# Performance work log

Measured on AMD Instinct MI355X. Metric: run time of the kernel, lower is better.

Reference implementation:

```python
import jax, jax.numpy as jnp
import numpy as np

B, LQ, LK, C = 16, 1024, 1024, 512
WH = int(LQ ** 0.5)  # 32


def setup_inputs() -> dict:
    key = jax.random.key(0)
    ks = jax.random.split(key, 6)
    s1 = 1.0 / np.sqrt(LK)
    return {
        "query": jax.random.normal(ks[0], (B, LQ, C), jnp.float32),
        "key": jax.random.normal(ks[1], (B, LK, C), jnp.float32),
        "value": jax.random.normal(ks[2], (B, LK, C), jnp.float32),
        # nn.Linear weights, stored [out_features, in_features] like torch
        "w1": jax.random.normal(ks[3], (LK, LK), jnp.float32) * s1,
        "w2": jax.random.normal(ks[4], (LK, LK), jnp.float32) * s1,
        "w3": jax.random.normal(ks[5], (1, LK), jnp.float32) * s1,
    }


def reference(query, key, value, w1, w2, w3):
    # cosine-similarity matrix (computed under no_grad in the original)
    q = query / 100.0
    k = key / 100.0
    qn = jnp.sqrt(jnp.sum(q * q, axis=-1))[:, :, None]   # [B, LQ, 1]
    kn = jnp.sqrt(jnp.sum(k * k, axis=-1))[:, None, :]   # [B, 1, LK]
    outer = qn * kn                                       # rank-1 outer product [B, LQ, LK]
    upper = jnp.einsum('bqc,bkc->bqk', q, k)              # [B, LQ, LK]
    similar_rev = jax.lax.stop_gradient(upper / (outer + 1e-6))

    # 3-layer MLP gating over the LK axis -> scalar weight per query row
    h = jax.nn.gelu(jnp.einsum('bqk,ok->bqo', similar_rev, w1), approximate=False)
    h = jax.nn.gelu(jnp.einsum('bqk,ok->bqo', h, w2), approximate=False)
    w = jnp.einsum('bqk,ok->bqo', h, w3)[..., 0]          # [B, LQ]

    # weight^T @ similar_rev / wh, then tanh -> per-key scalar gate [B, LK, 1]
    weight = jnp.einsum('bq,bqk->bk', w, similar_rev) / WH
    weight = jnp.tanh(weight)[:, :, None]

    # value modulation + residual
    return value * weight + value
```

## Files before the change

### kernel.cpp

```cpp
#include <hip/hip_runtime.h>
#include <hip/hip_bf16.h>

#define B_  16
#define LQ_ 1024
#define LK_ 1024
#define C_  512

typedef __attribute__((ext_vector_type(4))) float f32x4;
typedef __attribute__((ext_vector_type(8))) short bf16x8;

__device__ __forceinline__ float bf2f(ushort u) {
  union { unsigned int i; float f; } v; v.i = ((unsigned int)u) << 16; return v.f;
}
__device__ __forceinline__ ushort f2bf(float f) {
  union { float f; unsigned int i; } v; v.f = f;
  unsigned int r = v.i + 0x7fffu + ((v.i >> 16) & 1u);
  return (ushort)(r >> 16);
}
__device__ __forceinline__ float gelu_exact(float x) {
  return 0.5f * x * (1.0f + erff(x * 0.70710678118654752f));
}

__device__ __forceinline__ void gload_lds16(const ushort* g, ushort* l) {
  __builtin_amdgcn_global_load_lds(
      (const __attribute__((address_space(1))) void*)g,
      (__attribute__((address_space(3))) void*)l, 16, 0, 0);
}

__global__ __launch_bounds__(256) void prep_qk(const float* __restrict__ x,
                                               ushort* __restrict__ xb,
                                               float* __restrict__ norms) {
  int wid = blockIdx.x * 4 + (threadIdx.x >> 6);
  int lane = threadIdx.x & 63;
  const float* xr = x + (long)wid * C_;
  ushort* xo = xb + (long)wid * C_;
  float ss = 0.f;
#pragma unroll
  for (int i0 = 0; i0 < 2; ++i0) {
    int i = lane * 4 + i0 * 256;
    float4 v = *(const float4*)(xr + i);
    ss += v.x * v.x + v.y * v.y + v.z * v.z + v.w * v.w;
    ushort4 o;
    o.x = f2bf(v.x); o.y = f2bf(v.y); o.z = f2bf(v.z); o.w = f2bf(v.w);
    *(ushort4*)(xo + i) = o;
  }
#pragma unroll
  for (int off = 32; off > 0; off >>= 1) ss += __shfl_xor(ss, off);
  if (lane == 0) norms[wid] = sqrtf(ss);
}

__global__ __launch_bounds__(256) void conv_bf16(const float* __restrict__ x,
                                                 ushort* __restrict__ o, int n4) {
  int i = blockIdx.x * 256 + threadIdx.x;
  if (i < n4) {
    float4 v = *(const float4*)(x + (long)i * 4);
    ushort4 u;
    u.x = f2bf(v.x); u.y = f2bf(v.y); u.z = f2bf(v.z); u.w = f2bf(v.w);
    *(ushort4*)(o + (long)i * 4) = u;
  }
}

template <int EPI>
__global__ __launch_bounds__(512, 2) void gemm256(
    const ushort* __restrict__ A, const ushort* __restrict__ Bm,
    ushort* __restrict__ Cc, int K, long sA, long sB, long sC,
    const float* __restrict__ qn, const float* __restrict__ kn,
    const float* __restrict__ w3v, float* __restrict__ wv) {
  int per = (int)(gridDim.x >> 3);
  int orig = blockIdx.x;
  int id = (orig & 7) * per + (orig >> 3);
  int b = id >> 4;
  int rt = id & 15;
  const int bm = (rt >> 2) * 256, bn = (rt & 3) * 256;

  A += (long)b * sA;
  Bm += (long)b * sB;

  __shared__ ushort At[2][256][64];
  __shared__ ushort Bt[2][256][64];
  const int bufStride = 256 * 64;

  const int tid = threadIdx.x;
  const int lane = tid & 63, w = tid >> 6;
  const int wr = w >> 2, wc = w & 3;
  const int l16 = lane & 15, lhi = lane >> 4;

  f32x4 acc[8][4] = {};

  const ushort* gA[4];
  const ushort* gB[4];
  ushort* lA[4];
  ushort* lB[4];
#pragma unroll
  for (int i = 0; i < 4; ++i) {
    int c = i * 512 + tid;
    int row = c >> 3;
    int cb = (c & 7) ^ (row & 7);
    gA[i] = A + (long)(bm + row) * K + cb * 8;
    gB[i] = Bm + (long)(bn + row) * K + cb * 8;
    int wch = i * 512 + (tid & ~63);
    lA[i] = &At[0][0][0] + (size_t)wch * 8;
    lB[i] = &Bt[0][0][0] + (size_t)wch * 8;
  }

#pragma unroll
  for (int i = 0; i < 4; ++i) {
    gload_lds16(gA[i], lA[i]);
    gload_lds16(gB[i], lB[i]);
  }
  asm volatile("s_waitcnt vmcnt(0)" ::: "memory");
  __builtin_amdgcn_s_barrier();

  const int nt = K / 64;
  int cur = 0;
  for (int t = 0; t < nt; ++t) {
    const int koff = (t + 1) * 64;
    const bool pf = (t + 1 < nt);
    const ushort* Acur = &At[cur][0][0];
    const ushort* Bcur = &Bt[cur][0][0];
    const size_t nxo = (size_t)(cur ^ 1) * bufStride;

    bf16x8 bfr[4][2];

#pragma unroll
    for (int p = 0; p < 4; ++p) {
      bf16x8 af[2][2];
#pragma unroll
      for (int e = 0; e < 2; ++e)
#pragma unroll
        for (int kk = 0; kk < 2; ++kk) {
          int r = wr * 128 + (p * 2 + e) * 16 + l16;
          af[e][kk] = *(const bf16x8*)(Acur + r * 64 +
                                       (((kk * 4 + lhi) ^ (r & 7)) * 8));
        }
      if (p == 0) {
#pragma unroll
        for (int n = 0; n < 4; ++n)
#pragma unroll
          for (int kk = 0; kk < 2; ++kk) {
            int r = wc * 64 + n * 16 + l16;
            bfr[n][kk] = *(const bf16x8*)(Bcur + r * 64 +
                                          (((kk * 4 + lhi) ^ (r & 7)) * 8));
          }
      }
      if (pf) {
        if (p == 0) {
          gload_lds16(gA[0] + koff, lA[0] + nxo);
          gload_lds16(gA[1] + koff, lA[1] + nxo);
          gload_lds16(gB[0] + koff, lB[0] + nxo);
        } else if (p == 1) {
          gload_lds16(gA[2] + koff, lA[2] + nxo);
          gload_lds16(gA[3] + koff, lA[3] + nxo);
          gload_lds16(gB[1] + koff, lB[1] + nxo);
        } else if (p == 2) {
          gload_lds16(gB[2] + koff, lB[2] + nxo);
          gload_lds16(gB[3] + koff, lB[3] + nxo);
        }
      }
      __builtin_amdgcn_s_barrier();
      __builtin_amdgcn_s_setprio(1);
#pragma unroll
      for (int e = 0; e < 2; ++e)
#pragma unroll
        for (int n = 0; n < 4; ++n)
#pragma unroll
          for (int kk = 0; kk < 2; ++kk)
            acc[p * 2 + e][n] = __builtin_amdgcn_mfma_f32_16x16x32_bf16(
                af[e][kk], bfr[n][kk], acc[p * 2 + e][n], 0, 0, 0);
      __builtin_amdgcn_s_setprio(0);
      if (p == 3) asm volatile("s_waitcnt vmcnt(0)" ::: "memory");
      __builtin_amdgcn_s_barrier();
    }
    cur ^= 1;
  }

  if constexpr (EPI == 2) {
    float* wvb = wv + (long)b * LQ_;
    float w3c[4];
#pragma unroll
    for (int n = 0; n < 4; ++n) w3c[n] = w3v[bn + wc * 64 + n * 16 + l16];
#pragma unroll
    for (int m = 0; m < 8; ++m)
#pragma unroll
      for (int rr = 0; rr < 4; ++rr) {
        float s = 0.f;
#pragma unroll
        for (int n = 0; n < 4; ++n)
          s += gelu_exact(acc[m][n][rr]) * w3c[n];
        s += __shfl_xor(s, 1);
        s += __shfl_xor(s, 2);
        s += __shfl_xor(s, 4);
        s += __shfl_xor(s, 8);
        if (l16 == 0)
          atomicAdd(&wvb[bm + wr * 128 + m * 16 + lhi * 4 + rr], s);
      }
  } else {
    Cc += (long)b * sC;
    const float* qnb = qn + (long)b * LQ_;
    const float* knb = kn + (long)b * LK_;
#pragma unroll
    for (int m = 0; m < 8; ++m) {
      int row0 = bm + wr * 128 + m * 16 + lhi * 4;
#pragma unroll
      for (int n = 0; n < 4; ++n) {
        int col = bn + wc * 64 + n * 16 + l16;
#pragma unroll
        for (int rr = 0; rr < 4; ++rr) {
          float v = acc[m][n][rr];
          int grow = row0 + rr;
          if (EPI == 0) {
            v = v / (qnb[grow] * knb[col] + 1e-2f);
          } else {
            v = gelu_exact(v);
          }
          Cc[(long)grow * 1024 + col] = f2bf(v);
        }
      }
    }
  }
}

__global__ __launch_bounds__(256) void gate_partial(const ushort* __restrict__ S,
                                                    const float* __restrict__ wv,
                                                    float* __restrict__ wraw) {
  int b = blockIdx.z;
  int k = blockIdx.x * 256 + threadIdx.x;
  int q0 = blockIdx.y * 128;
  const ushort* Sb = S + (long)b * LQ_ * LK_;
  const float* wb = wv + b * LQ_;
  float acc = 0.f;
#pragma unroll 4
  for (int q = q0; q < q0 + 128; ++q) acc += wb[q] * bf2f(Sb[(long)q * LK_ + k]);
  atomicAdd(&wraw[b * LK_ + k], acc);
}

__global__ __launch_bounds__(256) void finalize(const float* __restrict__ value,
                                                const float* __restrict__ wraw,
                                                float* __restrict__ out) {
  long i = (long)blockIdx.x * 256 + threadIdx.x;
  long e = i * 4;
  int row = (int)(e >> 9);
  float g = 1.f + tanhf(wraw[row] * (1.f / 32.f));
  float4 v = ((const float4*)value)[i];
  v.x *= g; v.y *= g; v.z *= g; v.w *= g;
  ((float4*)out)[i] = v;
}

extern "C" void kernel_launch(void* const* d_in, const int* in_sizes, int n_in,
                              void* d_out, int out_size, void* d_ws,
                              size_t ws_size, hipStream_t stream) {
  const float* query = (const float*)d_in[0];
  const float* key   = (const float*)d_in[1];
  const float* value = (const float*)d_in[2];
  const float* w1    = (const float*)d_in[3];
  const float* w2    = (const float*)d_in[4];
  const float* w3    = (const float*)d_in[5];
  float* out = (float*)d_out;

  const size_t QB_BYTES = (size_t)B_ * LQ_ * C_ * 2;
  const size_t S_BYTES  = (size_t)B_ * LQ_ * LK_ * 2;
  const size_t W_BYTES  = (size_t)LK_ * LK_ * 2;
  const size_t OFF_QB = 0;
  const size_t OFF_KB = OFF_QB + QB_BYTES;
  const size_t OFF_S  = OFF_KB + QB_BYTES;
  const size_t OFF_H1 = OFF_S + S_BYTES;
  const size_t OFF_W1 = OFF_H1 + S_BYTES;
  const size_t OFF_W2 = OFF_W1 + W_BYTES;
  const size_t OFF_QN = OFF_W2 + W_BYTES;
  const size_t OFF_KN = OFF_QN + (size_t)B_ * LQ_ * 4;
  const size_t OFF_WV = OFF_KN + (size_t)B_ * LK_ * 4;
  const size_t OFF_WR = OFF_WV + (size_t)B_ * LQ_ * 4;
  const size_t TOTAL  = OFF_WR + (size_t)B_ * LK_ * 4;
  if (ws_size < TOTAL) return;

  char* ws = (char*)d_ws;
  ushort* Qb  = (ushort*)(ws + OFF_QB);
  ushort* Kb  = (ushort*)(ws + OFF_KB);
  ushort* S   = (ushort*)(ws + OFF_S);
  ushort* h1  = (ushort*)(ws + OFF_H1);
  ushort* W1b = (ushort*)(ws + OFF_W1);
  ushort* W2b = (ushort*)(ws + OFF_W2);
  float* qn   = (float*)(ws + OFF_QN);
  float* kn   = (float*)(ws + OFF_KN);
  float* wv   = (float*)(ws + OFF_WV);
  float* wraw = (float*)(ws + OFF_WR);

  prep_qk<<<dim3(B_ * LQ_ / 4), 256, 0, stream>>>(query, Qb, qn);
  prep_qk<<<dim3(B_ * LK_ / 4), 256, 0, stream>>>(key, Kb, kn);
  conv_bf16<<<dim3(LK_ * LK_ / 4 / 256), 256, 0, stream>>>(w1, W1b, LK_ * LK_ / 4);
  conv_bf16<<<dim3(LK_ * LK_ / 4 / 256), 256, 0, stream>>>(w2, W2b, LK_ * LK_ / 4);
  hipMemsetAsync(wraw, 0, (size_t)B_ * LK_ * 4, stream);
  hipMemsetAsync(wv, 0, (size_t)B_ * LQ_ * 4, stream);

  gemm256<0><<<dim3(256), 512, 0, stream>>>(
      Qb, Kb, S, C_, (long)LQ_ * C_, (long)LK_ * C_, (long)LQ_ * LK_,
      qn, kn, nullptr, nullptr);

  gemm256<1><<<dim3(256), 512, 0, stream>>>(
      S, W1b, h1, LK_, (long)LQ_ * LK_, 0L, (long)LQ_ * LK_,
      nullptr, nullptr, nullptr, nullptr);

  gemm256<2><<<dim3(256), 512, 0, stream>>>(
      h1, W2b, nullptr, LK_, (long)LQ_ * LK_, 0L, 0L,
      nullptr, nullptr, w3, wv);

  gate_partial<<<dim3(LK_ / 256, LQ_ / 128, B_), 256, 0, stream>>>(S, wv, wraw);

  finalize<<<dim3((size_t)B_ * LK_ * C_ / 4 / 256), 256, 0, stream>>>(value, wraw, out);
}
```

Before: 170.2 us.

## Restructure GEMM main loop into four quadrant phases with finer-grained prefetch waits

Rewrites the 256x256 bf16 GEMM inner loop into four MFMA quadrants per k-tile. Each quadrant issues a pair of global-to-LDS prefetches, and the vmcnt waits are staggered so later loads stay in flight across phases instead of draining fully each tile. B rows are remapped so each wave's two n-halves sit in separate 128-row LDS regions, allowing B fragments to be loaded in halves. The aim is to overlap global loads, LDS reads and MFMA work more tightly. In exchange it depends on subtle vmcnt accounting and barrier placement to stay correct, and the epilogue's acc-to-column mapping must match the new B row permutation.

Measured after the change: 166.2 us. -2.3%, faster.

```diff
diff --git a/kernel.cpp b/kernel.cpp
--- a/kernel.cpp
+++ b/kernel.cpp
@@ -73,12 +73,11 @@
   int rt = id & 15;
   const int bm = (rt >> 2) * 256, bn = (rt & 3) * 256;
 
-  A += (long)b * sA;
+  A += (long)b * sA + (long)bm * K;
   Bm += (long)b * sB;
 
-  __shared__ ushort At[2][256][64];
-  __shared__ ushort Bt[2][256][64];
-  const int bufStride = 256 * 64;
+  __shared__ ushort At[2][256 * 64];
+  __shared__ ushort Bt[2][256 * 64];
 
   const int tid = threadIdx.x;
   const int lane = tid & 63, w = tid >> 6;
@@ -87,92 +86,130 @@
 
   f32x4 acc[8][4] = {};
 
-  const ushort* gA[4];
-  const ushort* gB[4];
-  ushort* lA[4];
-  ushort* lB[4];
-#pragma unroll
-  for (int i = 0; i < 4; ++i) {
-    int c = i * 512 + tid;
-    int row = c >> 3;
-    int cb = (c & 7) ^ (row & 7);
-    gA[i] = A + (long)(bm + row) * K + cb * 8;
-    gB[i] = Bm + (long)(bn + row) * K + cb * 8;
-    int wch = i * 512 + (tid & ~63);
-    lA[i] = &At[0][0][0] + (size_t)wch * 8;
-    lB[i] = &Bt[0][0][0] + (size_t)wch * 8;
-  }
-
-#pragma unroll
-  for (int i = 0; i < 4; ++i) {
-    gload_lds16(gA[i], lA[i]);
-    gload_lds16(gB[i], lB[i]);
-  }
-  asm volatile("s_waitcnt vmcnt(0)" ::: "memory");
+  const ushort* gAs[4];
+  const ushort* gBs[4];
+  int dstc[4];
+#pragma unroll
+  for (int s = 0; s < 4; ++s) {
+    int c = s * 512 + tid;
+    int l = c >> 3;
+    int cb = (c & 7) ^ (l & 7);
+    gAs[s] = A + (long)l * K + cb * 8;
+    int nh = l >> 7, wcb = (l >> 5) & 3, jj = l & 31;
+    int rb = wcb * 64 + nh * 32 + jj;
+    gBs[s] = Bm + (long)(bn + rb) * K + cb * 8;
+    dstc[s] = (s * 512 + (tid & ~63)) * 8;
+  }
+
+  {
+    ushort* Ad = &At[0][0];
+    ushort* Bd = &Bt[0][0];
+    gload_lds16(gAs[0], Ad + dstc[0]);
+    gload_lds16(gAs[2], Ad + dstc[2]);
+    gload_lds16(gBs[0], Bd + dstc[0]);
+    gload_lds16(gBs[1], Bd + dstc[1]);
+    gload_lds16(gBs[2], Bd + dstc[2]);
+    gload_lds16(gBs[3], Bd + dstc[3]);
+    gload_lds16(gAs[1], Ad + dstc[1]);
+    gload_lds16(gAs[3], Ad + dstc[3]);
+  }
+  asm volatile("s_waitcnt vmcnt(4)" ::: "memory");
   __builtin_amdgcn_s_barrier();
+
+  const int xk0 = (lhi ^ (l16 & 7)) * 8;
+  const int xk1 = ((4 + lhi) ^ (l16 & 7)) * 8;
+
+#define MFMA_QUAD(MH, NH, BB)                                              \
+  __builtin_amdgcn_s_setprio(1);                                           \
+  _Pragma("unroll") for (int mi = 0; mi < 4; ++mi)                         \
+      _Pragma("unroll") for (int ni = 0; ni < 2; ++ni)                     \
+          _Pragma("unroll") for (int kk = 0; kk < 2; ++kk)                 \
+              acc[(MH)*4 + mi][(NH)*2 + ni] =                              \
+      __builtin_amdgcn_mfma_f32_16x16x32_bf16(                             \
+          aa[mi][kk], BB[ni][kk], acc[(MH)*4 + mi][(NH)*2 + ni], 0, 0, 0); \
+  __builtin_amdgcn_s_setprio(0);
 
   const int nt = K / 64;
   int cur = 0;
   for (int t = 0; t < nt; ++t) {
-    const int koff = (t + 1) * 64;
+    const ushort* Ac = &At[cur][0];
+    const ushort* Bc = &Bt[cur][0];
+    ushort* Ad = &At[cur ^ 1][0];
+    ushort* Bd = &Bt[cur ^ 1][0];
+    const int ko = (t + 1) * 64;
     const bool pf = (t + 1 < nt);
-    const ushort* Acur = &At[cur][0][0];
-    const ushort* Bcur = &Bt[cur][0][0];
-    const size_t nxo = (size_t)(cur ^ 1) * bufStride;
-
-    bf16x8 bfr[4][2];
-
-#pragma unroll
-    for (int p = 0; p < 4; ++p) {
-      bf16x8 af[2][2];
-#pragma unroll
-      for (int e = 0; e < 2; ++e)
-#pragma unroll
-        for (int kk = 0; kk < 2; ++kk) {
-          int r = wr * 128 + (p * 2 + e) * 16 + l16;
-          af[e][kk] = *(const bf16x8*)(Acur + r * 64 +
-                                       (((kk * 4 + lhi) ^ (r & 7)) * 8));
-        }
-      if (p == 0) {
-#pragma unroll
-        for (int n = 0; n < 4; ++n)
-#pragma unroll
-          for (int kk = 0; kk < 2; ++kk) {
-            int r = wc * 64 + n * 16 + l16;
-            bfr[n][kk] = *(const bf16x8*)(Bcur + r * 64 +
-                                          (((kk * 4 + lhi) ^ (r & 7)) * 8));
-          }
-      }
-      if (pf) {
-        if (p == 0) {
-          gload_lds16(gA[0] + koff, lA[0] + nxo);
-          gload_lds16(gA[1] + koff, lA[1] + nxo);
-          gload_lds16(gB[0] + koff, lB[0] + nxo);
-        } else if (p == 1) {
-          gload_lds16(gA[2] + koff, lA[2] + nxo);
-          gload_lds16(gA[3] + koff, lA[3] + nxo);
-          gload_lds16(gB[1] + koff, lB[1] + nxo);
-        } else if (p == 2) {
-          gload_lds16(gB[2] + koff, lB[2] + nxo);
-          gload_lds16(gB[3] + koff, lB[3] + nxo);
-        }
-      }
-      __builtin_amdgcn_s_barrier();
-      __builtin_amdgcn_s_setprio(1);
-#pragma unroll
-      for (int e = 0; e < 2; ++e)
-#pragma unroll
-        for (int n = 0; n < 4; ++n)
-#pragma unroll
-          for (int kk = 0; kk < 2; ++kk)
-            acc[p * 2 + e][n] = __builtin_amdgcn_mfma_f32_16x16x32_bf16(
-                af[e][kk], bfr[n][kk], acc[p * 2 + e][n], 0, 0, 0);
-      __builtin_amdgcn_s_setprio(0);
-      if (p == 3) asm volatile("s_waitcnt vmcnt(0)" ::: "memory");
-      __builtin_amdgcn_s_barrier();
-    }
+
+    bf16x8 aa[4][2], b0[2][2], b1[2][2];
+
+#pragma unroll
+    for (int mi = 0; mi < 4; ++mi) {
+      int r = wr * 128 + mi * 16 + l16;
+      aa[mi][0] = *(const bf16x8*)(Ac + r * 64 + xk0);
+      aa[mi][1] = *(const bf16x8*)(Ac + r * 64 + xk1);
+    }
+#pragma unroll
+    for (int ni = 0; ni < 2; ++ni) {
+      int lb = wc * 32 + ni * 16 + l16;
+      b0[ni][0] = *(const bf16x8*)(Bc + lb * 64 + xk0);
+      b0[ni][1] = *(const bf16x8*)(Bc + lb * 64 + xk1);
+    }
+    if (pf) {
+      gload_lds16(gAs[0] + ko, Ad + dstc[0]);
+      gload_lds16(gAs[2] + ko, Ad + dstc[2]);
+      asm volatile("s_waitcnt vmcnt(4)" ::: "memory");
+    } else {
+      asm volatile("s_waitcnt vmcnt(2)" ::: "memory");
+    }
+    __builtin_amdgcn_s_barrier();
+    asm volatile("s_waitcnt lgkmcnt(0)" ::: "memory");
+    __builtin_amdgcn_sched_barrier(0);
+    MFMA_QUAD(0, 0, b0)
+
+#pragma unroll
+    for (int ni = 0; ni < 2; ++ni) {
+      int lb = 128 + wc * 32 + ni * 16 + l16;
+      b1[ni][0] = *(const bf16x8*)(Bc + lb * 64 + xk0);
+      b1[ni][1] = *(const bf16x8*)(Bc + lb * 64 + xk1);
+    }
+    if (pf) {
+      gload_lds16(gBs[0] + ko, Bd + dstc[0]);
+      gload_lds16(gBs[1] + ko, Bd + dstc[1]);
+      asm volatile("s_waitcnt vmcnt(4)" ::: "memory");
+    } else {
+      asm volatile("s_waitcnt vmcnt(0)" ::: "memory");
+    }
+    __builtin_amdgcn_s_barrier();
+    asm volatile("s_waitcnt lgkmcnt(0)" ::: "memory");
+    __builtin_amdgcn_sched_barrier(0);
+    MFMA_QUAD(0, 1, b1)
+
+#pragma unroll
+    for (int mi = 0; mi < 4; ++mi) {
+      int r = wr * 128 + 64 + mi * 16 + l16;
+      aa[mi][0] = *(const bf16x8*)(Ac + r * 64 + xk0);
+      aa[mi][1] = *(const bf16x8*)(Ac + r * 64 + xk1);
+    }
+    if (pf) {
+      gload_lds16(gBs[2] + ko, Bd + dstc[2]);
+      gload_lds16(gBs[3] + ko, Bd + dstc[3]);
+      asm volatile("s_waitcnt vmcnt(4)" ::: "memory");
+    }
+    __builtin_amdgcn_s_barrier();
+    asm volatile("s_waitcnt lgkmcnt(0)" ::: "memory");
+    __builtin_amdgcn_sched_barrier(0);
+    MFMA_QUAD(1, 0, b0)
+
+    if (pf) {
+      gload_lds16(gAs[1] + ko, Ad + dstc[1]);
+      gload_lds16(gAs[3] + ko, Ad + dstc[3]);
+      asm volatile("s_waitcnt vmcnt(4)" ::: "memory");
+    }
+    __builtin_amdgcn_s_barrier();
+    MFMA_QUAD(1, 1, b1)
+
     cur ^= 1;
   }
+#undef MFMA_QUAD
 
   if constexpr (EPI == 2) {
     float* wvb = wv + (long)b * LQ_;
```
